# Performance work log

Measured on AMD Instinct MI355X. Metric: run time of the kernel, lower is better.

The kernel has to match this reference:

```python
import jax, jax.numpy as jnp
import numpy as np

N, E, IN_DIM, H, C = 100000, 1600000, 128, 4, 32
D = H * C  # 128


def setup_inputs() -> dict:
    key = jax.random.key(0)
    ks = jax.random.split(key, 8)
    rn = lambda k, shape, sc: (jax.random.normal(k, shape, jnp.float32) * sc)
    return {
        "x": rn(ks[0], (N, IN_DIM), 1.0),
        "edge_index": jax.random.randint(ks[1], (2, E), 0, N, jnp.int32),
        "lin_w": rn(ks[2], (IN_DIM, D), 0.05),
        "lin_b": jnp.zeros((D,), jnp.float32),
        "gat_w": rn(ks[3], (IN_DIM, D), 0.05),
        "att_src": rn(ks[4], (H, C), 0.1),
        "att_dst": rn(ks[5], (H, C), 0.1),
        "gat_bias": jnp.zeros((D,), jnp.float32),
        "bn_gamma": jnp.ones((D,), jnp.float32),
        "bn_beta": jnp.zeros((D,), jnp.float32),
    }


def reference(x, edge_index, lin_w, lin_b, gat_w, att_src, att_dst, gat_bias, bn_gamma, bn_beta):
    n = x.shape[0]
    heads, ch = att_src.shape
    # residual branch: h_in = Linear(x)
    h_in = x @ lin_w + lin_b  # [N, H*C]
    # GATConv: project, per-head attention logits
    xp = (x @ gat_w).reshape(n, heads, ch)  # [N, H, C]
    a_src = jnp.einsum("nhc,hc->nh", xp, att_src)  # [N, H]
    a_dst = jnp.einsum("nhc,hc->nh", xp, att_dst)  # [N, H]
    # PyG default add_self_loops=True
    loop = jnp.arange(n, dtype=edge_index.dtype)
    src = jnp.concatenate([edge_index[0], loop])  # message source j
    dst = jnp.concatenate([edge_index[1], loop])  # message target i
    e = jax.nn.leaky_relu(a_src[src] + a_dst[dst], 0.2)  # [E+N, H]
    # softmax over incoming edges per target node (stable, segment-wise)
    m = jax.ops.segment_max(e, dst, num_segments=n)
    ex = jnp.exp(e - m[dst])
    denom = jax.ops.segment_sum(ex, dst, num_segments=n)
    alpha = ex / denom[dst]  # [E+N, H]
    # attention-weighted aggregation (scatter-add)
    out = jax.ops.segment_sum(alpha[:, :, None] * xp[src], dst, num_segments=n)  # [N, H, C]
    h = out.reshape(n, heads * ch) + gat_bias  # concat heads + bias
    # BatchNorm1d (training-mode batch statistics, biased variance, eps=1e-5)
    mu = h.mean(axis=0)
    var = h.var(axis=0)
    h = (h - mu) / jnp.sqrt(var + 1e-5) * bn_gamma + bn_beta
    h = jax.nn.elu(h)
    return h_in + h
```

## Files before the change

### kernel.cpp

```cpp
#include <hip/hip_runtime.h>
#include <stdint.h>

typedef unsigned short u16;
typedef __attribute__((ext_vector_type(8))) short short8;
typedef __attribute__((ext_vector_type(4))) float floatx4;

#define DH 128
#define NH 4
#define CH 32

#define NPB  256
#define MAXB 512
#define EPB 8192
#define SGRID 512

__device__ __forceinline__ float bf2f(u16 u) {
    union { unsigned int i; float f; } c; c.i = ((unsigned int)u) << 16; return c.f;
}
__device__ __forceinline__ u16 f2bf(float f) {
    union { float f; unsigned int i; } c; c.f = f;
    unsigned int x = c.i;
    x += 0x7FFFu + ((x >> 16) & 1u);
    return (u16)(x >> 16);
}
__device__ __forceinline__ float b2f_lo(unsigned v) {
    union { unsigned u; float f; } c; c.u = v << 16; return c.f;
}
__device__ __forceinline__ float b2f_hi(unsigned v) {
    union { unsigned u; float f; } c; c.u = v & 0xffff0000u; return c.f;
}
__device__ __forceinline__ float lr(float x) { return fmaxf(x, 0.2f * x); }

__global__ void repack_w(const float* __restrict__ lin_w, const float* __restrict__ gat_w,
                         u16* __restrict__ wpack) {
    int t = blockIdx.x * blockDim.x + threadIdx.x;
    int j    = t & 7;
    int lane = (t >> 3) & 63;
    int ks   = (t >> 9) & 3;
    int ct   = t >> 11;
    int k    = ks * 32 + (lane >> 4) * 8 + j;
    int col  = ct * 16 + (lane & 15);
    float v = (col < DH) ? lin_w[k * DH + col] : gat_w[k * DH + (col - DH)];
    wpack[t] = f2bf(v);
}

__global__ __launch_bounds__(256) void gemm_mfma(
        const float* __restrict__ x, const float* __restrict__ lin_b,
        const u16* __restrict__ wpack, float* __restrict__ h_out,
        u16* __restrict__ xp, int N) {
    int wave = threadIdx.x >> 6;
    int lane = threadIdx.x & 63;
    int rowBase = blockIdx.x * 64 + wave * 16;
    if (rowBase >= N) return;
    int m = lane & 15, quad = lane >> 4;

    short8 afr[4];
    const float* xrow = x + (size_t)(rowBase + m) * DH + quad * 8;
    #pragma unroll
    for (int ks = 0; ks < 4; ks++) {
        float4 f0 = *(const float4*)(xrow + ks * 32);
        float4 f1 = *(const float4*)(xrow + ks * 32 + 4);
        short8 a;
        a[0] = (short)f2bf(f0.x); a[1] = (short)f2bf(f0.y);
        a[2] = (short)f2bf(f0.z); a[3] = (short)f2bf(f0.w);
        a[4] = (short)f2bf(f1.x); a[5] = (short)f2bf(f1.y);
        a[6] = (short)f2bf(f1.z); a[7] = (short)f2bf(f1.w);
        afr[ks] = a;
    }

    #pragma unroll 4
    for (int ct = 0; ct < 16; ct++) {
        floatx4 acc = {0.f, 0.f, 0.f, 0.f};
        const short8* bp = (const short8*)wpack + (ct * 4) * 64 + lane;
        #pragma unroll
        for (int ks = 0; ks < 4; ks++) {
            short8 bfr = bp[ks * 64];
            acc = __builtin_amdgcn_mfma_f32_16x16x32_bf16(afr[ks], bfr, acc, 0, 0, 0);
        }
        int col = ct * 16 + m;
        if (col < DH) {
            float bias = lin_b[col];
            #pragma unroll
            for (int r = 0; r < 4; r++)
                h_out[(size_t)(rowBase + quad * 4 + r) * DH + col] = acc[r] + bias;
        } else {
            int c2 = col - DH;
            #pragma unroll
            for (int r = 0; r < 4; r++)
                xp[(size_t)(rowBase + quad * 4 + r) * DH + c2] = f2bf(acc[r]);
        }
    }
}

__global__ __launch_bounds__(256) void att_kernel(
        const u16* __restrict__ xp, const float* __restrict__ att_src,
        const float* __restrict__ att_dst, float* __restrict__ a_src,
        float* __restrict__ a_dst, int N) {
    int t = blockIdx.x * blockDim.x + threadIdx.x;
    if (t >= N * NH) return;
    int h = t & 3;
    const short8* v = (const short8*)(xp + (size_t)t * CH);
    const float* ws = att_src + h * CH;
    const float* wd = att_dst + h * CH;
    float s = 0.f, d = 0.f;
    #pragma unroll
    for (int b = 0; b < 4; b++) {
        short8 a = v[b];
        #pragma unroll
        for (int j = 0; j < 8; j++) {
            float xv = bf2f((u16)a[j]);
            s = fmaf(xv, ws[b * 8 + j], s);
            d = fmaf(xv, wd[b * 8 + j], d);
        }
    }
    a_src[t] = s;
    a_dst[t] = d;
}


__global__ __launch_bounds__(256) void bucket_count(
        const int* __restrict__ ei, int E, int N, int B,
        int* __restrict__ bcount) {
    __shared__ int h[MAXB];
    for (int j = threadIdx.x; j < B; j += 256) h[j] = 0;
    __syncthreads();
    int i0 = blockIdx.x * EPB;
    int i1 = min(E, i0 + EPB);
    for (int i = i0 + threadIdx.x; i < i1; i += 256) {
        int d = min(max(ei[E + i], 0), N - 1);
        atomicAdd(&h[d >> 8], 1);
    }
    __syncthreads();
    for (int j = threadIdx.x; j < B; j += 256) {
        int c = h[j];
        if (c) atomicAdd(&bcount[j], c);
    }
}

__global__ __launch_bounds__(512) void bucket_scan(
        const int* __restrict__ bcount, int B,
        int* __restrict__ bbase, int* __restrict__ bcur) {
    __shared__ int buf[512];
    int t = threadIdx.x;
    int v = (t < B) ? bcount[t] : 0;
    buf[t] = v;
    __syncthreads();
    for (int s = 1; s < 512; s <<= 1) {
        int add = (t >= s) ? buf[t - s] : 0;
        __syncthreads();
        buf[t] += add;
        __syncthreads();
    }
    if (t < B) { int e = buf[t] - v; bbase[t] = e; bcur[t] = e; }
}

__global__ __launch_bounds__(256) void bucket_scatter(
        const int* __restrict__ ei, int E, int N, int B,
        int* __restrict__ bcur, unsigned* __restrict__ tmp) {
    __shared__ int h[MAXB];
    __shared__ int base[MAXB];
    for (int j = threadIdx.x; j < B; j += 256) h[j] = 0;
    __syncthreads();
    int i0 = blockIdx.x * EPB;
    int i1 = min(E, i0 + EPB);
    for (int i = i0 + threadIdx.x; i < i1; i += 256) {
        int d = min(max(ei[E + i], 0), N - 1);
        atomicAdd(&h[d >> 8], 1);
    }
    __syncthreads();
    for (int j = threadIdx.x; j < B; j += 256) {
        int c = h[j];
        base[j] = c ? atomicAdd(&bcur[j], c) : 0;
    }
    __syncthreads();
    for (int j = threadIdx.x; j < B; j += 256) h[j] = 0;
    __syncthreads();
    for (int i = i0 + threadIdx.x; i < i1; i += 256) {
        int s = min(max(ei[i], 0), N - 1);
        int d = min(max(ei[E + i], 0), N - 1);
        int b = d >> 8;
        int pos = base[b] + atomicAdd(&h[b], 1);
        tmp[pos] = (unsigned)s | ((unsigned)(d & 255) << 17);
    }
}

__global__ __launch_bounds__(256) void bucket_to_csr(
        const unsigned* __restrict__ tmp, const int* __restrict__ bbase,
        const int* __restrict__ bcount, int N,
        int* __restrict__ offsets, int* __restrict__ deg,
        int* __restrict__ col) {
    __shared__ int cnt[NPB];
    __shared__ int excl[NPB];
    int b = blockIdx.x;
    int t = threadIdx.x;
    int bstart = bbase[b];
    int c = bcount[b];
    cnt[t] = 0;
    __syncthreads();
    for (int k = t; k < c; k += 256) {
        unsigned pk = tmp[bstart + k];
        atomicAdd(&cnt[pk >> 17], 1);
    }
    __syncthreads();
    int v = cnt[t];
    excl[t] = v;
    __syncthreads();
    for (int s = 1; s < 256; s <<= 1) {
        int add = (t >= s) ? excl[t - s] : 0;
        __syncthreads();
        excl[t] += add;
        __syncthreads();
    }
    int mystart = excl[t] - v;
    int node = b * NPB + t;
    if (node < N) {
        offsets[node] = bstart + mystart;
        deg[node] = v;
    }
    cnt[t] = mystart;
    __syncthreads();
    for (int k = t; k < c; k += 256) {
        unsigned pk = tmp[bstart + k];
        int slot = atomicAdd(&cnt[pk >> 17], 1);
        col[bstart + slot] = (int)(pk & 0x1FFFFu);
    }
}

__global__ __launch_bounds__(256) void csr_gather(
        const int* __restrict__ offsets, const int* __restrict__ deg,
        const int* __restrict__ col, const float* __restrict__ a_src,
        const float* __restrict__ a_dst, const u16* __restrict__ xp,
        float* __restrict__ agg, int N) {
    int node = blockIdx.x * 4 + (threadIdx.x >> 6);
    if (node >= N) return;
    int lane  = threadIdx.x & 63;
    int h     = lane >> 4;
    int q     = lane & 3;
    int esl   = lane >> 2;
    int lane2 = lane << 1;

    float ad_q = a_dst[node * NH + q];

    float w = __expf(lr(a_src[node * NH + h] + a_dst[node * NH + h]));
    unsigned xv = *(const unsigned*)(xp + (size_t)node * DH + lane2);
    float acc0 = w * b2f_lo(xv);
    float acc1 = w * b2f_hi(xv);
    float denv = 0.f;

    int off = offsets[node], dg = deg[node];
    const int* cp = col + off;

#define EDGE_F(K) {                                                       \
        float e = __shfl(ev, ((K) << 2) | h, 64);                         \
        int  su = __builtin_amdgcn_readlane(s_e, (K) << 2);               \
        const u16* row = xp + ((size_t)(unsigned)su << 7);                \
        unsigned v = *(const unsigned*)(row + lane2);                     \
        acc0 = fmaf(e, b2f_lo(v), acc0);                                  \
        acc1 = fmaf(e, b2f_hi(v), acc1); }

#define EDGE_P(K) {                                                       \
        float e = ((K) < rem) ? __shfl(ev, ((K) << 2) | h, 64) : 0.f;     \
        int  su = __builtin_amdgcn_readlane(s_e, (K) << 2);               \
        const u16* row = xp + ((size_t)(unsigned)su << 7);                \
        unsigned v = *(const unsigned*)(row + lane2);                     \
        acc0 = fmaf(e, b2f_lo(v), acc0);                                  \
        acc1 = fmaf(e, b2f_hi(v), acc1); }

    for (int k0 = 0; k0 < dg; k0 += 16) {
        int rem  = dg - k0;
        int kidx = min(k0 + esl, dg - 1);
        int s_e  = cp[kidx];
        float ev = __expf(lr(a_src[s_e * NH + q] + ad_q));
        denv += ((k0 + esl) < dg) ? ev : 0.f;
        if (rem >= 16) {
            #pragma unroll
            for (int k = 0; k < 16; k++) EDGE_F(k)
        } else {
            #pragma unroll
            for (int k = 0; k < 16; k++) EDGE_P(k)
        }
    }
#undef EDGE_F
#undef EDGE_P

    #pragma unroll
    for (int m = 4; m <= 32; m <<= 1)
        denv += __shfl_xor(denv, m, 64);
    float den = __shfl(denv, h, 64) + w;

    float inv = 1.0f / den;
    float2 o; o.x = acc0 * inv; o.y = acc1 * inv;
    *(float2*)(agg + (size_t)node * DH + lane2) = o;
}

__global__ __launch_bounds__(256) void stats_kernel(
        const float* __restrict__ agg, int N,
        float* __restrict__ colsum, float* __restrict__ colsumsq) {
    int grp = threadIdx.x & 31;
    int sub = threadIdx.x >> 5;
    int c4  = grp << 2;
    floatx4 s1 = {0.f, 0.f, 0.f, 0.f}, s2 = {0.f, 0.f, 0.f, 0.f};
    int rpb = (N + gridDim.x - 1) / gridDim.x;
    int r0  = blockIdx.x * rpb;
    int r1  = min(N, r0 + rpb);
    for (int r = r0 + sub; r < r1; r += 8) {
        floatx4 v = *(const floatx4*)(agg + (size_t)r * DH + c4);
        s1 += v;
        s2 += v * v;
    }
    __shared__ floatx4 red1[8][32];
    __shared__ floatx4 red2[8][32];
    red1[sub][grp] = s1;
    red2[sub][grp] = s2;
    __syncthreads();
    for (int s = 4; s >= 1; s >>= 1) {
        if (sub < s) {
            red1[sub][grp] += red1[sub + s][grp];
            red2[sub][grp] += red2[sub + s][grp];
        }
        __syncthreads();
    }
    if (sub == 0) {
        floatx4 a1 = red1[0][grp];
        floatx4 a2 = red2[0][grp];
        #pragma unroll
        for (int j = 0; j < 4; j++) {
            atomicAdd(&colsum[c4 + j],   a1[j]);
            atomicAdd(&colsumsq[c4 + j], a2[j]);
        }
    }
}

__global__ __launch_bounds__(256) void final_kernel(
        const float* __restrict__ agg, const float* __restrict__ colsum,
        const float* __restrict__ colsumsq, const float* __restrict__ gamma,
        const float* __restrict__ beta, float* __restrict__ out, int N) {
    int t = blockIdx.x * blockDim.x + threadIdx.x;
    if (t >= N * (DH / 4)) return;
    int row = t >> 5;
    int c4  = (t & 31) << 2;
    float inv_n = 1.0f / (float)N;

    floatx4 s1 = *(const floatx4*)(colsum   + c4);
    floatx4 s2 = *(const floatx4*)(colsumsq + c4);
    floatx4 g  = *(const floatx4*)(gamma    + c4);
    floatx4 b  = *(const floatx4*)(beta     + c4);
    floatx4 a  = *(const floatx4*)(agg + (size_t)row * DH + c4);
    floatx4 o  = *(const floatx4*)(out + (size_t)row * DH + c4);

    #pragma unroll
    for (int j = 0; j < 4; j++) {
        float mu   = s1[j] * inv_n;
        float var  = s2[j] * inv_n - mu * mu;
        float rstd = rsqrtf(var + 1e-5f);
        float v = (a[j] - mu) * rstd * g[j] + b[j];
        v = v > 0.f ? v : (__expf(v) - 1.f);
        float r = o[j] + v;
        if (!(r >= -1e30f && r <= 1e30f)) r = 512.0f;
        o[j] = r;
    }
    *(floatx4*)(out + (size_t)row * DH + c4) = o;
}

extern "C" void kernel_launch(void* const* d_in, const int* in_sizes, int n_in,
                              void* d_out, int out_size, void* d_ws, size_t ws_size,
                              hipStream_t stream) {
    const float* x        = (const float*)d_in[0];
    const int*   ei       = (const int*)d_in[1];
    const float* lin_w    = (const float*)d_in[2];
    const float* lin_b    = (const float*)d_in[3];
    const float* gat_w    = (const float*)d_in[4];
    const float* att_src  = (const float*)d_in[5];
    const float* att_dst  = (const float*)d_in[6];
    const float* bn_gamma = (const float*)d_in[8];
    const float* bn_beta  = (const float*)d_in[9];

    int N = in_sizes[0] / DH;
    int E = in_sizes[1] / 2;
    int B = (N + NPB - 1) / NPB;
    int EB = (E + EPB - 1) / EPB;

    char* p = (char*)d_ws;
    u16*   xp      = (u16*)p;        p += (size_t)N * DH * 2;
    float* a_src   = (float*)p;      p += (size_t)N * NH * 4;
    float* a_dst   = (float*)p;      p += (size_t)N * NH * 4;
    u16*   wpack   = (u16*)p;        p += 32768 * 2;
    int*   col     = (int*)p;        p += (size_t)E * 4;
    int*   offsets = (int*)p;        p += (size_t)N * 4;
    int*   deg     = (int*)p;        p += (size_t)N * 4;
    int*   bbase   = (int*)p;        p += MAXB * 4;
    int*   bcur    = (int*)p;        p += MAXB * 4;
    char* zero_begin = p;
    int*   bcount  = (int*)p;        p += MAXB * 4;
    float* colsum  = (float*)p;      p += DH * 4;
    float* colsumsq= (float*)p;      p += DH * 4;
    size_t zero_bytes = (size_t)(p - zero_begin);
    float* agg     = (float*)p;
    unsigned* tmp  = (unsigned*)agg;

    hipMemsetAsync(zero_begin, 0, zero_bytes, stream);

    repack_w<<<(16 * 4 * 64 * 8) / 256, 256, 0, stream>>>(lin_w, gat_w, wpack);

    gemm_mfma<<<(N + 63) / 64, 256, 0, stream>>>(x, lin_b, wpack,
                                                 (float*)d_out, xp, N);

    att_kernel<<<(N * NH + 255) / 256, 256, 0, stream>>>(xp, att_src, att_dst,
                                                         a_src, a_dst, N);

    bucket_count<<<EB, 256, 0, stream>>>(ei, E, N, B, bcount);
    bucket_scan<<<1, 512, 0, stream>>>(bcount, B, bbase, bcur);
    bucket_scatter<<<EB, 256, 0, stream>>>(ei, E, N, B, bcur, tmp);
    bucket_to_csr<<<B, 256, 0, stream>>>(tmp, bbase, bcount, N,
                                         offsets, deg, col);

    csr_gather<<<(N + 3) / 4, 256, 0, stream>>>(offsets, deg, col, a_src,
                                                a_dst, xp, agg, N);
    stats_kernel<<<SGRID, 256, 0, stream>>>(agg, N, colsum, colsumsq);
    final_kernel<<<(N * (DH / 4) + 255) / 256, 256, 0, stream>>>(
        agg, colsum, colsumsq, bn_gamma, bn_beta, (float*)d_out, N);
}
```

Before: 374.1 us.

## Fuse attention logits into GEMM epilogue and BN stats into gather

The attention-logit computation now happens in the GEMM epilogue: per-head dot products run on the MFMA accumulators, are reduced with cross-lane shuffles, and the separate att_kernel pass that re-read xp is removed. The CSR gather becomes a persistent grid-stride kernel (fixed grid of 2048 blocks) that also accumulates per-column sum and sum-of-squares, so the stats_kernel pass over agg is gone. Logits are now taken from fp32 accumulators rather than the bf16-rounded xp, which shifts numerics slightly. The persistent gather may lose some load balance or occupancy in exchange for fewer kernel launches and less memory traffic.

```diff
diff --git a/kernel.cpp b/kernel.cpp
--- a/kernel.cpp
+++ b/kernel.cpp
@@ -12,7 +12,7 @@
 #define NPB  256
 #define MAXB 512
 #define EPB 8192
-#define SGRID 512
+#define GGRID 2048
 
 __device__ __forceinline__ float bf2f(u16 u) {
     union { unsigned int i; float f; } c; c.i = ((unsigned int)u) << 16; return c.f;
@@ -46,8 +46,10 @@
 
 __global__ __launch_bounds__(256) void gemm_mfma(
         const float* __restrict__ x, const float* __restrict__ lin_b,
-        const u16* __restrict__ wpack, float* __restrict__ h_out,
-        u16* __restrict__ xp, int N) {
+        const u16* __restrict__ wpack, const float* __restrict__ att_src,
+        const float* __restrict__ att_dst, float* __restrict__ h_out,
+        u16* __restrict__ xp, float* __restrict__ a_src,
+        float* __restrict__ a_dst, int N) {
     int wave = threadIdx.x >> 6;
     int lane = threadIdx.x & 63;
     int rowBase = blockIdx.x * 64 + wave * 16;
@@ -69,7 +71,7 @@
     }
 
     #pragma unroll 4
-    for (int ct = 0; ct < 16; ct++) {
+    for (int ct = 0; ct < 8; ct++) {
         floatx4 acc = {0.f, 0.f, 0.f, 0.f};
         const short8* bp = (const short8*)wpack + (ct * 4) * 64 + lane;
         #pragma unroll
@@ -78,43 +80,59 @@
             acc = __builtin_amdgcn_mfma_f32_16x16x32_bf16(afr[ks], bfr, acc, 0, 0, 0);
         }
         int col = ct * 16 + m;
-        if (col < DH) {
-            float bias = lin_b[col];
+        float bias = lin_b[col];
+        #pragma unroll
+        for (int r = 0; r < 4; r++)
+            h_out[(size_t)(rowBase + quad * 4 + r) * DH + col] = acc[r] + bias;
+    }
+
+    float pS[4], pD[4];
+    #pragma unroll
+    for (int ct2 = 0; ct2 < 8; ct2++) {
+        const int ct = ct2 + 8;
+        const int hh = ct2 >> 1;
+        floatx4 acc = {0.f, 0.f, 0.f, 0.f};
+        const short8* bp = (const short8*)wpack + (ct * 4) * 64 + lane;
+        #pragma unroll
+        for (int ks = 0; ks < 4; ks++) {
+            short8 bfr = bp[ks * 64];
+            acc = __builtin_amdgcn_mfma_f32_16x16x32_bf16(afr[ks], bfr, acc, 0, 0, 0);
+        }
+        int c2 = ct2 * 16 + m;
+        #pragma unroll
+        for (int r = 0; r < 4; r++)
+            xp[(size_t)(rowBase + quad * 4 + r) * DH + c2] = f2bf(acc[r]);
+
+        int ch = ((ct2 & 1) << 4) + m;
+        float ws = att_src[hh * CH + ch];
+        float wd = att_dst[hh * CH + ch];
+        if (!(ct2 & 1)) {
             #pragma unroll
-            for (int r = 0; r < 4; r++)
-                h_out[(size_t)(rowBase + quad * 4 + r) * DH + col] = acc[r] + bias;
+            for (int r = 0; r < 4; r++) { pS[r] = acc[r] * ws; pD[r] = acc[r] * wd; }
         } else {
-            int c2 = col - DH;
             #pragma unroll
-            for (int r = 0; r < 4; r++)
-                xp[(size_t)(rowBase + quad * 4 + r) * DH + c2] = f2bf(acc[r]);
+            for (int r = 0; r < 4; r++) {
+                pS[r] = fmaf(acc[r], ws, pS[r]);
+                pD[r] = fmaf(acc[r], wd, pD[r]);
+            }
+            #pragma unroll
+            for (int r = 0; r < 4; r++) {
+                #pragma unroll
+                for (int mk = 1; mk <= 8; mk <<= 1) {
+                    pS[r] += __shfl_xor(pS[r], mk, 64);
+                    pD[r] += __shfl_xor(pD[r], mk, 64);
+                }
+            }
+            if (m == 0) {
+                #pragma unroll
+                for (int r = 0; r < 4; r++) {
+                    int node = rowBase + quad * 4 + r;
+                    a_src[node * NH + hh] = pS[r];
+                    a_dst[node * NH + hh] = pD[r];
+                }
+            }
         }
     }
-}
-
-__global__ __launch_bounds__(256) void att_kernel(
-        const u16* __restrict__ xp, const float* __restrict__ att_src,
-        const float* __restrict__ att_dst, float* __restrict__ a_src,
-        float* __restrict__ a_dst, int N) {
-    int t = blockIdx.x * blockDim.x + threadIdx.x;
-    if (t >= N * NH) return;
-    int h = t & 3;
-    const short8* v = (const short8*)(xp + (size_t)t * CH);
-    const float* ws = att_src + h * CH;
-    const float* wd = att_dst + h * CH;
-    float s = 0.f, d = 0.f;
-    #pragma unroll
-    for (int b = 0; b < 4; b++) {
-        short8 a = v[b];
-        #pragma unroll
-        for (int j = 0; j < 8; j++) {
-            float xv = bf2f((u16)a[j]);
-            s = fmaf(xv, ws[b * 8 + j], s);
-            d = fmaf(xv, wd[b * 8 + j], d);
-        }
-    }
-    a_src[t] = s;
-    a_dst[t] = d;
 }
 
 
@@ -230,25 +248,30 @@
         const int* __restrict__ offsets, const int* __restrict__ deg,
         const int* __restrict__ col, const float* __restrict__ a_src,
         const float* __restrict__ a_dst, const u16* __restrict__ xp,
-        float* __restrict__ agg, int N) {
-    int node = blockIdx.x * 4 + (threadIdx.x >> 6);
-    if (node >= N) return;
+        float* __restrict__ agg, float* __restrict__ colsum,
+        float* __restrict__ colsumsq, int N) {
+    int wave  = threadIdx.x >> 6;
     int lane  = threadIdx.x & 63;
     int h     = lane >> 4;
     int q     = lane & 3;
     int esl   = lane >> 2;
     int lane2 = lane << 1;
 
-    float ad_q = a_dst[node * NH + q];
-
-    float w = __expf(lr(a_src[node * NH + h] + a_dst[node * NH + h]));
-    unsigned xv = *(const unsigned*)(xp + (size_t)node * DH + lane2);
-    float acc0 = w * b2f_lo(xv);
-    float acc1 = w * b2f_hi(xv);
-    float denv = 0.f;
-
-    int off = offsets[node], dg = deg[node];
-    const int* cp = col + off;
+    float s1x = 0.f, s1y = 0.f, s2x = 0.f, s2y = 0.f;
+
+    for (int base = blockIdx.x * 4; base < N; base += gridDim.x * 4) {
+        int node = base + wave;
+        if (node < N) {
+            float ad_q = a_dst[node * NH + q];
+
+            float w = __expf(lr(a_src[node * NH + h] + a_dst[node * NH + h]));
+            unsigned xv = *(const unsigned*)(xp + (size_t)node * DH + lane2);
+            float acc0 = w * b2f_lo(xv);
+            float acc1 = w * b2f_hi(xv);
+            float denv = 0.f;
+
+            int off = offsets[node], dg = deg[node];
+            const int* cp = col + off;
 
 #define EDGE_F(K) {                                                       \
         float e = __shfl(ev, ((K) << 2) | h, 64);                         \
@@ -266,68 +289,50 @@
         acc0 = fmaf(e, b2f_lo(v), acc0);                                  \
         acc1 = fmaf(e, b2f_hi(v), acc1); }
 
-    for (int k0 = 0; k0 < dg; k0 += 16) {
-        int rem  = dg - k0;
-        int kidx = min(k0 + esl, dg - 1);
-        int s_e  = cp[kidx];
-        float ev = __expf(lr(a_src[s_e * NH + q] + ad_q));
-        denv += ((k0 + esl) < dg) ? ev : 0.f;
-        if (rem >= 16) {
-            #pragma unroll
-            for (int k = 0; k < 16; k++) EDGE_F(k)
-        } else {
-            #pragma unroll
-            for (int k = 0; k < 16; k++) EDGE_P(k)
-        }
-    }
+            for (int k0 = 0; k0 < dg; k0 += 16) {
+                int rem  = dg - k0;
+                int kidx = min(k0 + esl, dg - 1);
+                int s_e  = cp[kidx];
+                float ev = __expf(lr(a_src[s_e * NH + q] + ad_q));
+                denv += ((k0 + esl) < dg) ? ev : 0.f;
+                if (rem >= 16) {
+                    #pragma unroll
+                    for (int k = 0; k < 16; k++) EDGE_F(k)
+                } else {
+                    #pragma unroll
+                    for (int k = 0; k < 16; k++) EDGE_P(k)
+                }
+            }
 #undef EDGE_F
 #undef EDGE_P
 
-    #pragma unroll
-    for (int m = 4; m <= 32; m <<= 1)
-        denv += __shfl_xor(denv, m, 64);
-    float den = __shfl(denv, h, 64) + w;
-
-    float inv = 1.0f / den;
-    float2 o; o.x = acc0 * inv; o.y = acc1 * inv;
-    *(float2*)(agg + (size_t)node * DH + lane2) = o;
-}
-
-__global__ __launch_bounds__(256) void stats_kernel(
-        const float* __restrict__ agg, int N,
-        float* __restrict__ colsum, float* __restrict__ colsumsq) {
-    int grp = threadIdx.x & 31;
-    int sub = threadIdx.x >> 5;
-    int c4  = grp << 2;
-    floatx4 s1 = {0.f, 0.f, 0.f, 0.f}, s2 = {0.f, 0.f, 0.f, 0.f};
-    int rpb = (N + gridDim.x - 1) / gridDim.x;
-    int r0  = blockIdx.x * rpb;
-    int r1  = min(N, r0 + rpb);
-    for (int r = r0 + sub; r < r1; r += 8) {
-        floatx4 v = *(const floatx4*)(agg + (size_t)r * DH + c4);
-        s1 += v;
-        s2 += v * v;
-    }
-    __shared__ floatx4 red1[8][32];
-    __shared__ floatx4 red2[8][32];
-    red1[sub][grp] = s1;
-    red2[sub][grp] = s2;
-    __syncthreads();
-    for (int s = 4; s >= 1; s >>= 1) {
-        if (sub < s) {
-            red1[sub][grp] += red1[sub + s][grp];
-            red2[sub][grp] += red2[sub + s][grp];
+            #pragma unroll
+            for (int mm = 4; mm <= 32; mm <<= 1)
+                denv += __shfl_xor(denv, mm, 64);
+            float den = __shfl(denv, h, 64) + w;
+
+            float inv = 1.0f / den;
+            float ox = acc0 * inv, oy = acc1 * inv;
+            float2 o; o.x = ox; o.y = oy;
+            *(float2*)(agg + (size_t)node * DH + lane2) = o;
+            s1x += ox; s1y += oy;
+            s2x += ox * ox; s2y += oy * oy;
         }
-        __syncthreads();
-    }
-    if (sub == 0) {
-        floatx4 a1 = red1[0][grp];
-        floatx4 a2 = red2[0][grp];
-        #pragma unroll
-        for (int j = 0; j < 4; j++) {
-            atomicAdd(&colsum[c4 + j],   a1[j]);
-            atomicAdd(&colsumsq[c4 + j], a2[j]);
-        }
+    }
+
+    __shared__ float red[4][64][4];
+    red[wave][lane][0] = s1x; red[wave][lane][1] = s1y;
+    red[wave][lane][2] = s2x; red[wave][lane][3] = s2y;
+    __syncthreads();
+    if (wave == 0) {
+        float a0 = red[0][lane][0] + red[1][lane][0] + red[2][lane][0] + red[3][lane][0];
+        float a1 = red[0][lane][1] + red[1][lane][1] + red[2][lane][1] + red[3][lane][1];
+        float a2 = red[0][lane][2] + red[1][lane][2] + red[2][lane][2] + red[3][lane][2];
+        float a3 = red[0][lane][3] + red[1][lane][3] + red[2][lane][3] + red[3][lane][3];
+        atomicAdd(&colsum[lane2],       a0);
+        atomicAdd(&colsum[lane2 + 1],   a1);
+        atomicAdd(&colsumsq[lane2],     a2);
+        atomicAdd(&colsumsq[lane2 + 1], a3);
     }
 }
 
@@ -402,11 +407,9 @@
 
     repack_w<<<(16 * 4 * 64 * 8) / 256, 256, 0, stream>>>(lin_w, gat_w, wpack);
 
-    gemm_mfma<<<(N + 63) / 64, 256, 0, stream>>>(x, lin_b, wpack,
-                                                 (float*)d_out, xp, N);
-
-    att_kernel<<<(N * NH + 255) / 256, 256, 0, stream>>>(xp, att_src, att_dst,
-                                                         a_src, a_dst, N);
+    gemm_mfma<<<(N + 63) / 64, 256, 0, stream>>>(x, lin_b, wpack, att_src,
+                                                 att_dst, (float*)d_out, xp,
+                                                 a_src, a_dst, N);
 
     bucket_count<<<EB, 256, 0, stream>>>(ei, E, N, B, bcount);
     bucket_scan<<<1, 512, 0, stream>>>(bcount, B, bbase, bcur);
@@ -414,9 +417,8 @@
     bucket_to_csr<<<B, 256, 0, stream>>>(tmp, bbase, bcount, N,
                                          offsets, deg, col);
 
-    csr_gather<<<(N + 3) / 4, 256, 0, stream>>>(offsets, deg, col, a_src,
-                                                a_dst, xp, agg, N);
-    stats_kernel<<<SGRID, 256, 0, stream>>>(agg, N, colsum, colsumsq);
+    csr_gather<<<GGRID, 256, 0, stream>>>(offsets, deg, col, a_src, a_dst,
+                                          xp, agg, colsum, colsumsq, N);
     final_kernel<<<(N * (DH / 4) + 255) / 256, 256, 0, stream>>>(
         agg, colsum, colsumsq, bn_gamma, bn_beta, (float*)d_out, N);
 }
```

New measurement: 401.0 us. 1.07x slower.
